# Optimization experiments

Hardware: AMD Instinct MI355X
Metric: run time of the kernel (lower is better)

The kernel has to match this reference:

```python
import jax, jax.numpy as jnp
import numpy as np

N_NODES = 50000
BN_EPS = 1e-5


def graph_conv(x, row, col, ew, n):
    # deg from source indices only (matches torch.bincount(row))
    deg = jnp.zeros((n,), x.dtype).at[row].add(1.0)
    dinv = jnp.where(deg > 0, deg ** -0.5, 0.0)
    norm = dinv[row] * ew * dinv[col]                     # [E]
    msg = norm[:, None] * x[row]                          # [E, F]
    return jax.ops.segment_sum(msg, col, num_segments=n)  # out[dst] += w * x[src]


def batch_norm(x, gamma, beta):
    # training-mode BN over the node (batch) dim, biased variance
    mu = jnp.mean(x, axis=0)
    var = jnp.mean((x - mu) ** 2, axis=0)
    return (x - mu) / jnp.sqrt(var + BN_EPS) * gamma + beta


def setup_inputs() -> dict:
    key = jax.random.key(0)
    ks = jax.random.split(key, 12)
    node_features = jax.random.normal(ks[0], (N_NODES, 100), dtype=jnp.float32)
    edge_index = jax.random.randint(ks[1], (2, 800000), 0, N_NODES, dtype=jnp.int64)
    edge_weights = jax.random.uniform(ks[2], (800000,), dtype=jnp.float32)
    def lin(k, fi, fo):
        lim = 1.0 / np.sqrt(fi)
        k1, k2 = jax.random.split(k)
        W = jax.random.uniform(k1, (fi, fo), minval=-lim, maxval=lim, dtype=jnp.float32)
        b = jax.random.uniform(k2, (fo,), minval=-lim, maxval=lim, dtype=jnp.float32)
        return W, b
    W0, b0 = lin(ks[3], 100, 128)
    W1, b1 = lin(ks[4], 128, 128)
    W2, b2 = lin(ks[5], 128, 64)
    return {
        "node_features": node_features, "edge_index": edge_index, "edge_weights": edge_weights,
        "W0": W0, "b0": b0, "g0": jnp.ones((128,), jnp.float32), "be0": jnp.zeros((128,), jnp.float32),
        "W1": W1, "b1": b1, "g1": jnp.ones((128,), jnp.float32), "be1": jnp.zeros((128,), jnp.float32),
        "W2": W2, "b2": b2,
    }


def reference(node_features, edge_index, edge_weights,
              W0, b0, g0, be0, W1, b1, g1, be1, W2, b2):
    n = node_features.shape[0]
    row, col = edge_index[0], edge_index[1]
    x = node_features
    # layer 0
    x = graph_conv(x, row, col, edge_weights, n)
    x = jax.nn.relu(batch_norm(x @ W0 + b0, g0, be0))
    # layer 1
    x = graph_conv(x, row, col, edge_weights, n)
    x = jax.nn.relu(batch_norm(x @ W1 + b1, g1, be1))
    # final layer (no BN/relu)
    x = graph_conv(x, row, col, edge_weights, n)
    return x @ W2 + b2
```

## Files before the change

kernel.cpp:

```cpp
#include <hip/hip_runtime.h>
#include <cstdint>

#define F0 100
#define FH 128
#define FO 64
#define BN_EPS 1e-5f

typedef unsigned short ushort_t;
typedef unsigned int uint_t;

static inline int ceil_div(long long a, long long b) { return (int)((a + b - 1) / b); }

__device__ __forceinline__ float bf_lo(uint_t w) { return __uint_as_float(w << 16); }
__device__ __forceinline__ float bf_hi(uint_t w) { return __uint_as_float(w & 0xffff0000u); }
__device__ __forceinline__ uint_t f2bf(float f) {
  uint_t u = __float_as_uint(f);
  return (u + 0x7fffu + ((u >> 16) & 1u)) >> 16;
}
__device__ __forceinline__ uint_t pack2(float a, float b) {
  return f2bf(a) | (f2bf(b) << 16);
}


template <int K, int F, int TM, bool BN_A, bool A_BF16, bool OUT_BF16>
__device__ __forceinline__ void gemm2_body(int bid, const void* __restrict__ A_,
                                           const float* __restrict__ W,
                                           const float* __restrict__ bias,
                                           const float* __restrict__ scA,
                                           const float* __restrict__ shA,
                                           void* __restrict__ out_, int n) {
  constexpr int NCG = F / 4;
  constexpr int NRG = 256 / NCG;
  constexpr int BR = NRG * TM;
  constexpr int BK = 32;
  constexpr int F4 = F / 4;

  __shared__ float sW[BK][F];
  __shared__ float sA[BR][BK];

  const int tid = threadIdx.x;
  const int cg = tid % NCG;
  const int rg = tid / NCG;
  const int row0 = bid * BR;

  float4 acc[TM];
#pragma unroll
  for (int t = 0; t < TM; ++t) acc[t] = make_float4(0.f, 0.f, 0.f, 0.f);

  const float4* W4 = (const float4*)W;
  const float4 z4 = make_float4(0.f, 0.f, 0.f, 0.f);

  for (int k0 = 0; k0 < K; k0 += BK) {
    for (int i = tid; i < BK * F4; i += 256) {
      int kk = i / F4, f4 = i % F4;
      int gk = k0 + kk;
      ((float4*)&sW[kk][0])[f4] = (gk < K) ? W4[(size_t)gk * F4 + f4] : z4;
    }
    for (int i = tid; i < BR * (BK / 4); i += 256) {
      int r = i / (BK / 4), k4 = i % (BK / 4);
      int gr = row0 + r;
      int gk = k0 + k4 * 4;
      float4 av = z4;
      if (gr < n && gk + 3 < K) {
        if (A_BF16) {
          uint2 u = ((const uint2*)A_)[(size_t)gr * (K / 4) + (gk >> 2)];
          av.x = bf_lo(u.x); av.y = bf_hi(u.x);
          av.z = bf_lo(u.y); av.w = bf_hi(u.y);
        } else {
          av = ((const float4*)A_)[(size_t)gr * (K / 4) + (gk >> 2)];
        }
        if (BN_A) {
          float4 sc = ((const float4*)scA)[gk >> 2];
          float4 sh = ((const float4*)shA)[gk >> 2];
          av.x = fmaxf(fmaf(av.x, sc.x, sh.x), 0.f);
          av.y = fmaxf(fmaf(av.y, sc.y, sh.y), 0.f);
          av.z = fmaxf(fmaf(av.z, sc.z, sh.z), 0.f);
          av.w = fmaxf(fmaf(av.w, sc.w, sh.w), 0.f);
        }
      }
      ((float4*)&sA[r][0])[k4] = av;
    }
    __syncthreads();
#pragma unroll 4
    for (int kk = 0; kk < BK; ++kk) {
      float4 w = ((const float4*)&sW[kk][0])[cg];
#pragma unroll
      for (int t = 0; t < TM; ++t) {
        float a = sA[rg * TM + t][kk];
        acc[t].x = fmaf(a, w.x, acc[t].x);
        acc[t].y = fmaf(a, w.y, acc[t].y);
        acc[t].z = fmaf(a, w.z, acc[t].z);
        acc[t].w = fmaf(a, w.w, acc[t].w);
      }
    }
    __syncthreads();
  }

  float4 bb = bias ? ((const float4*)bias)[cg] : z4;
#pragma unroll
  for (int t = 0; t < TM; ++t) {
    int gr = row0 + rg * TM + t;
    if (gr < n) {
      float4 v = acc[t];
      v.x += bb.x; v.y += bb.y; v.z += bb.z; v.w += bb.w;
      if (OUT_BF16) {
        ((uint2*)out_)[(size_t)gr * F4 + cg] = make_uint2(pack2(v.x, v.y), pack2(v.z, v.w));
      } else {
        ((float4*)out_)[(size_t)gr * F4 + cg] = v;
      }
    }
  }
}

template <int K, int F, int TM, bool BN_A, bool A_BF16, bool OUT_BF16>
__global__ __launch_bounds__(256) void gemm2_kernel(const void* __restrict__ A,
                                                    const float* __restrict__ W,
                                                    const float* __restrict__ bias,
                                                    const float* __restrict__ scA,
                                                    const float* __restrict__ shA,
                                                    void* __restrict__ out, int n) {
  gemm2_body<K, F, TM, BN_A, A_BF16, OUT_BF16>(blockIdx.x, A, W, bias, scA, shA, out, n);
}


__global__ __launch_bounds__(256) void hist_pos_kernel(const int* __restrict__ row,
                                                       const int* __restrict__ col,
                                                       int* __restrict__ degr,
                                                       int* __restrict__ degc,
                                                       int* __restrict__ posw, int E) {
  int e = blockIdx.x * blockDim.x + threadIdx.x;
  if (e >= E) return;
  atomicAdd(&degr[row[e]], 1);
  posw[e] = atomicAdd(&degc[col[e]], 1);
}


__global__ __launch_bounds__(256) void scan_fused_kernel(const int* __restrict__ degr,
                                                         const int* __restrict__ degc,
                                                         float* __restrict__ dinv,
                                                         int* __restrict__ startp,
                                                         int* __restrict__ bsums, int n) {
  __shared__ int s[256];
  int i = blockIdx.x * 256 + threadIdx.x;
  int dc = 0;
  if (i < n) {
    int dr = degr[i];
    dc = degc[i];
    dinv[i] = (dr > 0) ? rsqrtf((float)dr) : 0.0f;
  }
  s[threadIdx.x] = dc;
  __syncthreads();
  for (int off = 1; off < 256; off <<= 1) {
    int t = 0;
    if (threadIdx.x >= off) t = s[threadIdx.x - off];
    __syncthreads();
    if (threadIdx.x >= off) s[threadIdx.x] += t;
    __syncthreads();
  }
  if (i < n) startp[i] = s[threadIdx.x] - dc;
  if (threadIdx.x == 255) bsums[blockIdx.x] = s[255];
}

__global__ __launch_bounds__(256) void scan_partials_kernel(int* __restrict__ bsums, int nb) {
  __shared__ int s[256];
  int v = (threadIdx.x < nb) ? bsums[threadIdx.x] : 0;
  s[threadIdx.x] = v;
  __syncthreads();
  for (int off = 1; off < 256; off <<= 1) {
    int t = 0;
    if (threadIdx.x >= off) t = s[threadIdx.x - off];
    __syncthreads();
    if (threadIdx.x >= off) s[threadIdx.x] += t;
    __syncthreads();
  }
  if (threadIdx.x < nb) bsums[threadIdx.x] = s[threadIdx.x] - v;
}


__global__ __launch_bounds__(256) void fused_scatter_gemm_kernel(
    const int* __restrict__ row, const int* __restrict__ col, const float* __restrict__ ew,
    const float* __restrict__ dinv, const int* __restrict__ startp,
    const int* __restrict__ bsums, const int* __restrict__ posw, int2* __restrict__ ep, int E,
    const float* __restrict__ A, const float* __restrict__ W, void* __restrict__ out, int n,
    int GB) {
  int bid = blockIdx.x;
  int r5 = bid % 5;
  int g = bid / 5;
  if (r5 == 0 && g < GB) {
    gemm2_body<F0, FH, 8, false, false, true>(g, A, W, nullptr, nullptr, nullptr, out, n);
    return;
  }
  int h = (r5 == 0) ? (bid - GB) : (bid - (g + 1));
  int e = h * 256 + threadIdx.x;
  if (e >= E) return;
  int r = row[e], c = col[e];
  int pos = startp[c] + bsums[c >> 8] + posw[e];
  float coef = dinv[r] * ew[e] * dinv[c];
  ep[pos] = make_int2(r, __float_as_int(coef));
}


template <int F, bool DO_BN, bool OUT_F32>
__global__ __launch_bounds__(256) void conv_bf16_kernel(const ushort_t* __restrict__ x,
                                                        const int* __restrict__ startp,
                                                        const int* __restrict__ bsums,
                                                        const int* __restrict__ degc,
                                                        const int2* __restrict__ ep,
                                                        const float* __restrict__ bias,
                                                        const float* __restrict__ scale,
                                                        const float* __restrict__ shift,
                                                        void* __restrict__ out, int n, int E) {
  constexpr int G2 = F / 8;
  constexpr int TPD = G2 / 2;
  constexpr int DPB = 256 / TPD;
  constexpr int CHUNK = 1024;
  __shared__ int2 eps[CHUNK];

  const int d0 = blockIdx.x * DPB;
  const int dst = d0 + threadIdx.x / TPD;
  const int q = threadIdx.x % TPD;
  const bool valid = dst < n;

  const int blkStart = startp[d0] + bsums[d0 >> 8];
  const int dEnd0 = (d0 + DPB < n) ? (d0 + DPB) : n;
  const int blkEnd = (dEnd0 < n) ? (startp[dEnd0] + bsums[dEnd0 >> 8]) : E;

  int s0 = 0, myEnd = 0;
  if (valid) {
    s0 = startp[dst] + bsums[dst >> 8];
    myEnd = s0 + degc[dst];
  }

  const uint4* x4 = (const uint4*)x;

  float sc[16], sh[16];
  if (DO_BN) {
#pragma unroll
    for (int ch = 0; ch < 2; ++ch) {
      int g = q + ch * TPD;
#pragma unroll
      for (int j = 0; j < 8; ++j) {
        sc[ch * 8 + j] = scale[g * 8 + j];
        sh[ch * 8 + j] = shift[g * 8 + j];
      }
    }
  }

  float acc[16];
#pragma unroll
  for (int j = 0; j < 16; ++j) acc[j] = 0.f;

  for (int cb = blkStart; cb < blkEnd; cb += CHUNK) {
    int cnt = min(CHUNK, blkEnd - cb);
    if (cb != blkStart) __syncthreads();
    for (int i = threadIdx.x; i < cnt; i += 256) eps[i] = ep[cb + i];
    __syncthreads();
    if (valid) {
      int k0 = max(s0, cb);
      int k1 = min(myEnd, cb + cnt);
      for (int k = k0; k < k1; ++k) {
        int2 e = eps[k - cb];
        float c = __int_as_float(e.y);
        const uint4* xp = x4 + (size_t)e.x * G2 + q;
        uint4 v0 = xp[0];
        uint4 v1 = xp[TPD];
        uint_t vv[8] = {v0.x, v0.y, v0.z, v0.w, v1.x, v1.y, v1.z, v1.w};
#pragma unroll
        for (int hh = 0; hh < 8; ++hh) {
          float f0 = bf_lo(vv[hh]);
          float f1 = bf_hi(vv[hh]);
          if (DO_BN) {
            f0 = fmaxf(fmaf(f0, sc[2 * hh], sh[2 * hh]), 0.f);
            f1 = fmaxf(fmaf(f1, sc[2 * hh + 1], sh[2 * hh + 1]), 0.f);
          }
          acc[2 * hh] = fmaf(c, f0, acc[2 * hh]);
          acc[2 * hh + 1] = fmaf(c, f1, acc[2 * hh + 1]);
        }
      }
    }
  }

  if (!valid) return;

  if (bias) {
#pragma unroll
    for (int ch = 0; ch < 2; ++ch) {
      int g = q + ch * TPD;
#pragma unroll
      for (int j = 0; j < 8; ++j) acc[ch * 8 + j] += bias[g * 8 + j];
    }
  }

  if (OUT_F32) {
    float4* o4 = (float4*)out;
    size_t base = (size_t)dst * (F / 4);
    o4[base + 2 * q] = make_float4(acc[0], acc[1], acc[2], acc[3]);
    o4[base + 2 * q + 1] = make_float4(acc[4], acc[5], acc[6], acc[7]);
    o4[base + 2 * (q + TPD)] = make_float4(acc[8], acc[9], acc[10], acc[11]);
    o4[base + 2 * (q + TPD) + 1] = make_float4(acc[12], acc[13], acc[14], acc[15]);
  } else {
    uint4* o4 = (uint4*)out;
    size_t base = (size_t)dst * G2;
    o4[base + q] = make_uint4(pack2(acc[0], acc[1]), pack2(acc[2], acc[3]),
                              pack2(acc[4], acc[5]), pack2(acc[6], acc[7]));
    o4[base + q + TPD] = make_uint4(pack2(acc[8], acc[9]), pack2(acc[10], acc[11]),
                                    pack2(acc[12], acc[13]), pack2(acc[14], acc[15]));
  }
}


__global__ __launch_bounds__(128) void bn_stats_fin_kernel(const ushort_t* __restrict__ z,
                                                           float* __restrict__ sum,
                                                           float* __restrict__ sumsq,
                                                           const float* __restrict__ g,
                                                           const float* __restrict__ be,
                                                           float* __restrict__ scale,
                                                           float* __restrict__ shift,
                                                           int n, int* __restrict__ ctr) {
  int f = threadIdx.x;
  float s = 0.0f, s2 = 0.0f;
  for (int r = blockIdx.x; r < n; r += gridDim.x) {
    float v = __uint_as_float(((uint_t)z[(size_t)r * FH + f]) << 16);
    s += v;
    s2 += v * v;
  }
  unsafeAtomicAdd(&sum[f], s);
  unsafeAtomicAdd(&sumsq[f], s2);
  __threadfence();
  __syncthreads();
  __shared__ int lastFlag;
  if (f == 0) lastFlag = (atomicAdd(ctr, 1) == (int)gridDim.x - 1) ? 1 : 0;
  __syncthreads();
  if (lastFlag) {
    float S = atomicAdd(&sum[f], 0.0f);
    float S2 = atomicAdd(&sumsq[f], 0.0f);
    float invN = 1.0f / (float)n;
    float mean = S * invN;
    float var = fmaxf(S2 * invN - mean * mean, 0.0f);
    float sc = g[f] / sqrtf(var + BN_EPS);
    scale[f] = sc;
    shift[f] = be[f] - mean * sc;
  }
}


extern "C" void kernel_launch(void* const* d_in, const int* in_sizes, int n_in,
                              void* d_out, int out_size, void* d_ws, size_t ws_size,
                              hipStream_t stream) {
  const float* x   = (const float*)d_in[0];
  const int*   ei  = (const int*)d_in[1];
  const float* ew  = (const float*)d_in[2];
  const float* W0  = (const float*)d_in[3];
  const float* b0  = (const float*)d_in[4];
  const float* g0  = (const float*)d_in[5];
  const float* be0 = (const float*)d_in[6];
  const float* W1  = (const float*)d_in[7];
  const float* b1  = (const float*)d_in[8];
  const float* g1  = (const float*)d_in[9];
  const float* be1 = (const float*)d_in[10];
  const float* W2  = (const float*)d_in[11];
  const float* b2  = (const float*)d_in[12];

  const int n = in_sizes[0] / F0;
  const int E = in_sizes[2];
  const int* row = ei;
  const int* col = ei + E;

  ushort_t* bufA  = (ushort_t*)d_ws;
  ushort_t* bufB  = bufA + (size_t)n * FH;
  int2*   ep      = (int2*)(bufB + (size_t)n * FH);
  int*    degc    = (int*)(ep + E);
  int*    degr    = degc + n;
  float*  sum0    = (float*)(degr + n);
  float*  sumsq0  = sum0 + FH;
  float*  sum1    = sumsq0 + FH;
  float*  sumsq1  = sum1 + FH;
  int*    ctr     = (int*)(sumsq1 + FH);
  const size_t zero_bytes = (2 * (size_t)n + 4 * FH + 2) * 4;
  int*    startp  = ctr + 2;
  float*  dinv    = (float*)(startp + n);
  int*    bsums   = (int*)(dinv + n);
  float*  scale0  = (float*)(bsums + 256);
  float*  shift0  = scale0 + FH;
  float*  scale1  = shift0 + FH;
  float*  shift1  = scale1 + FH;
  int*    posw    = (int*)bufB;

  const int nb = ceil_div(n, 256);
  const int GB = ceil_div(n, 64);
  const int HB = ceil_div(E, 256);
  const int CB_H = ceil_div(n, 32);
  const int CB_O = ceil_div(n, 64);

  (void)hipMemsetAsync(degc, 0, zero_bytes, stream);
  hist_pos_kernel<<<HB, 256, 0, stream>>>(row, col, degr, degc, posw, E);
  scan_fused_kernel<<<nb, 256, 0, stream>>>(degr, degc, dinv, startp, bsums, n);
  scan_partials_kernel<<<1, 256, 0, stream>>>(bsums, nb);
  fused_scatter_gemm_kernel<<<GB + HB, 256, 0, stream>>>(row, col, ew, dinv, startp, bsums,
                                                         posw, ep, E, x, W0, bufA, n, GB);

  conv_bf16_kernel<FH, false, false><<<CB_H, 256, 0, stream>>>(
      bufA, startp, bsums, degc, ep, b0, nullptr, nullptr, bufB, n, E);
  bn_stats_fin_kernel<<<256, 128, 0, stream>>>(bufB, sum0, sumsq0, g0, be0, scale0, shift0,
                                               n, ctr + 0);

  conv_bf16_kernel<FH, true, false><<<CB_H, 256, 0, stream>>>(
      bufB, startp, bsums, degc, ep, nullptr, scale0, shift0, bufA, n, E);
  gemm2_kernel<FH, FH, 8, false, true, true><<<GB, 256, 0, stream>>>(
      bufA, W1, b1, nullptr, nullptr, bufB, n);
  bn_stats_fin_kernel<<<256, 128, 0, stream>>>(bufB, sum1, sumsq1, g1, be1, scale1, shift1,
                                               n, ctr + 1);

  gemm2_kernel<FH, FO, 4, true, true, true><<<GB, 256, 0, stream>>>(
      bufB, W2, nullptr, scale1, shift1, bufA, n);
  conv_bf16_kernel<FO, false, true><<<CB_O, 256, 0, stream>>>(
      bufA, startp, bsums, degc, ep, b2, nullptr, nullptr, (float*)d_out, n, E);
}
```

Measured before the change: 406.2 us.

## Fuse aggregation with following GEMM and pad degree counters to reduce contention

New measurement: 409.7 us. About the same (+0.9%).

```diff
diff --git a/kernel.cpp b/kernel.cpp
--- a/kernel.cpp
+++ b/kernel.cpp
@@ -4,6 +4,7 @@
 #define F0 100
 #define FH 128
 #define FO 64
+#define PD 4
 #define BN_EPS 1e-5f
 
 typedef unsigned short ushort_t;
@@ -22,17 +23,14 @@
 }
 
 
-template <int K, int F, int TM, bool BN_A, bool A_BF16, bool OUT_BF16>
+template <int K, int F, int TM, int BK, bool A_BF16, bool OUT_BF16>
 __device__ __forceinline__ void gemm2_body(int bid, const void* __restrict__ A_,
                                            const float* __restrict__ W,
                                            const float* __restrict__ bias,
-                                           const float* __restrict__ scA,
-                                           const float* __restrict__ shA,
                                            void* __restrict__ out_, int n) {
   constexpr int NCG = F / 4;
   constexpr int NRG = 256 / NCG;
   constexpr int BR = NRG * TM;
-  constexpr int BK = 32;
   constexpr int F4 = F / 4;
 
   __shared__ float sW[BK][F];
@@ -69,14 +67,6 @@
         } else {
           av = ((const float4*)A_)[(size_t)gr * (K / 4) + (gk >> 2)];
         }
-        if (BN_A) {
-          float4 sc = ((const float4*)scA)[gk >> 2];
-          float4 sh = ((const float4*)shA)[gk >> 2];
-          av.x = fmaxf(fmaf(av.x, sc.x, sh.x), 0.f);
-          av.y = fmaxf(fmaf(av.y, sc.y, sh.y), 0.f);
-          av.z = fmaxf(fmaf(av.z, sc.z, sh.z), 0.f);
-          av.w = fmaxf(fmaf(av.w, sc.w, sh.w), 0.f);
-        }
       }
       ((float4*)&sA[r][0])[k4] = av;
     }
@@ -112,31 +102,28 @@
   }
 }
 
-template <int K, int F, int TM, bool BN_A, bool A_BF16, bool OUT_BF16>
-__global__ __launch_bounds__(256) void gemm2_kernel(const void* __restrict__ A,
-                                                    const float* __restrict__ W,
-                                                    const float* __restrict__ bias,
-                                                    const float* __restrict__ scA,
-                                                    const float* __restrict__ shA,
-                                                    void* __restrict__ out, int n) {
-  gemm2_body<K, F, TM, BN_A, A_BF16, OUT_BF16>(blockIdx.x, A, W, bias, scA, shA, out, n);
-}
-
-
-__global__ __launch_bounds__(256) void hist_pos_kernel(const int* __restrict__ row,
-                                                       const int* __restrict__ col,
-                                                       int* __restrict__ degr,
-                                                       int* __restrict__ degc,
-                                                       int* __restrict__ posw, int E) {
-  int e = blockIdx.x * blockDim.x + threadIdx.x;
+
+__global__ __launch_bounds__(256) void fused_gemm_hist_kernel(
+    const float* __restrict__ A, const float* __restrict__ W, void* __restrict__ out, int n,
+    int GB, const int* __restrict__ row, const int* __restrict__ col,
+    int* __restrict__ degr_p, int* __restrict__ degc_p, int* __restrict__ posw, int E) {
+  int bid = blockIdx.x;
+  int r5 = bid % 5;
+  int g = bid / 5;
+  if (r5 == 0 && g < GB) {
+    gemm2_body<F0, FH, 8, 16, false, true>(g, A, W, nullptr, out, n);
+    return;
+  }
+  int h = (r5 == 0) ? (bid - GB) : (bid - (g + 1));
+  int e = h * 256 + threadIdx.x;
   if (e >= E) return;
-  atomicAdd(&degr[row[e]], 1);
-  posw[e] = atomicAdd(&degc[col[e]], 1);
-}
-
-
-__global__ __launch_bounds__(256) void scan_fused_kernel(const int* __restrict__ degr,
-                                                         const int* __restrict__ degc,
+  atomicAdd(&degr_p[(size_t)row[e] * PD], 1);
+  posw[e] = atomicAdd(&degc_p[(size_t)col[e] * PD], 1);
+}
+
+
+__global__ __launch_bounds__(256) void scan_fused_kernel(const int* __restrict__ degr_p,
+                                                         const int* __restrict__ degc_p,
                                                          float* __restrict__ dinv,
                                                          int* __restrict__ startp,
                                                          int* __restrict__ bsums, int n) {
@@ -144,8 +131,8 @@
   int i = blockIdx.x * 256 + threadIdx.x;
   int dc = 0;
   if (i < n) {
-    int dr = degr[i];
-    dc = degc[i];
+    int dr = degr_p[(size_t)i * PD];
+    dc = degc_p[(size_t)i * PD];
     dinv[i] = (dr > 0) ? rsqrtf((float)dr) : 0.0f;
   }
   s[threadIdx.x] = dc;
@@ -177,21 +164,15 @@
 }
 
 
-__global__ __launch_bounds__(256) void fused_scatter_gemm_kernel(
-    const int* __restrict__ row, const int* __restrict__ col, const float* __restrict__ ew,
-    const float* __restrict__ dinv, const int* __restrict__ startp,
-    const int* __restrict__ bsums, const int* __restrict__ posw, int2* __restrict__ ep, int E,
-    const float* __restrict__ A, const float* __restrict__ W, void* __restrict__ out, int n,
-    int GB) {
-  int bid = blockIdx.x;
-  int r5 = bid % 5;
-  int g = bid / 5;
-  if (r5 == 0 && g < GB) {
-    gemm2_body<F0, FH, 8, false, false, true>(g, A, W, nullptr, nullptr, nullptr, out, n);
-    return;
-  }
-  int h = (r5 == 0) ? (bid - GB) : (bid - (g + 1));
-  int e = h * 256 + threadIdx.x;
+__global__ __launch_bounds__(256) void csr_scatter2_kernel(const int* __restrict__ row,
+                                                           const int* __restrict__ col,
+                                                           const float* __restrict__ ew,
+                                                           const float* __restrict__ dinv,
+                                                           const int* __restrict__ startp,
+                                                           const int* __restrict__ bsums,
+                                                           const int* __restrict__ posw,
+                                                           int2* __restrict__ ep, int E) {
+  int e = blockIdx.x * blockDim.x + threadIdx.x;
   if (e >= E) return;
   int r = row[e], c = col[e];
   int pos = startp[c] + bsums[c >> 8] + posw[e];
@@ -200,37 +181,14 @@
 }
 
 
-template <int F, bool DO_BN, bool OUT_F32>
-__global__ __launch_bounds__(256) void conv_bf16_kernel(const ushort_t* __restrict__ x,
-                                                        const int* __restrict__ startp,
-                                                        const int* __restrict__ bsums,
-                                                        const int* __restrict__ degc,
-                                                        const int2* __restrict__ ep,
-                                                        const float* __restrict__ bias,
-                                                        const float* __restrict__ scale,
-                                                        const float* __restrict__ shift,
-                                                        void* __restrict__ out, int n, int E) {
-  constexpr int G2 = F / 8;
-  constexpr int TPD = G2 / 2;
-  constexpr int DPB = 256 / TPD;
-  constexpr int CHUNK = 1024;
-  __shared__ int2 eps[CHUNK];
-
-  const int d0 = blockIdx.x * DPB;
-  const int dst = d0 + threadIdx.x / TPD;
-  const int q = threadIdx.x % TPD;
-  const bool valid = dst < n;
-
-  const int blkStart = startp[d0] + bsums[d0 >> 8];
-  const int dEnd0 = (d0 + DPB < n) ? (d0 + DPB) : n;
-  const int blkEnd = (dEnd0 < n) ? (startp[dEnd0] + bsums[dEnd0 >> 8]) : E;
-
-  int s0 = 0, myEnd = 0;
-  if (valid) {
-    s0 = startp[dst] + bsums[dst >> 8];
-    myEnd = s0 + degc[dst];
-  }
-
+template <bool DO_BN>
+__device__ __forceinline__ void conv_accum_128(const ushort_t* __restrict__ x, int s0, int d,
+                                               int q, const int2* __restrict__ ep,
+                                               const float* __restrict__ scale,
+                                               const float* __restrict__ shift,
+                                               float* __restrict__ acc) {
+  constexpr int G2 = FH / 8;
+  constexpr int TPD = 8;
   const uint4* x4 = (const uint4*)x;
 
   float sc[16], sh[16];
@@ -245,66 +203,142 @@
       }
     }
   }
-
+#pragma unroll
+  for (int j = 0; j < 16; ++j) acc[j] = 0.f;
+
+  for (int k = 0; k < d; ++k) {
+    int2 e = ep[s0 + k];
+    float c = __int_as_float(e.y);
+    const uint4* xp = x4 + (size_t)e.x * G2 + q;
+    uint4 v0 = xp[0];
+    uint4 v1 = xp[TPD];
+    uint_t vv[8] = {v0.x, v0.y, v0.z, v0.w, v1.x, v1.y, v1.z, v1.w};
+#pragma unroll
+    for (int hh = 0; hh < 8; ++hh) {
+      float f0 = bf_lo(vv[hh]);
+      float f1 = bf_hi(vv[hh]);
+      if (DO_BN) {
+        f0 = fmaxf(fmaf(f0, sc[2 * hh], sh[2 * hh]), 0.f);
+        f1 = fmaxf(fmaf(f1, sc[2 * hh + 1], sh[2 * hh + 1]), 0.f);
+      }
+      acc[2 * hh] = fmaf(c, f0, acc[2 * hh]);
+      acc[2 * hh + 1] = fmaf(c, f1, acc[2 * hh + 1]);
+    }
+  }
+}
+
+
+__global__ __launch_bounds__(256) void conv0_kernel(const ushort_t* __restrict__ x,
+                                                    const int* __restrict__ startp,
+                                                    const int* __restrict__ bsums,
+                                                    const int* __restrict__ degc_p,
+                                                    const int2* __restrict__ ep,
+                                                    const float* __restrict__ bias,
+                                                    ushort_t* __restrict__ out, int n) {
+  constexpr int TPD = 8;
+  long long tid = (long long)blockIdx.x * 256 + threadIdx.x;
+  if (tid >= (long long)n * TPD) return;
+  int dst = (int)(tid / TPD);
+  int q = (int)(tid % TPD);
+  int s0 = startp[dst] + bsums[dst >> 8];
+  int d = degc_p[(size_t)dst * PD];
   float acc[16];
-#pragma unroll
-  for (int j = 0; j < 16; ++j) acc[j] = 0.f;
-
-  for (int cb = blkStart; cb < blkEnd; cb += CHUNK) {
-    int cnt = min(CHUNK, blkEnd - cb);
-    if (cb != blkStart) __syncthreads();
-    for (int i = threadIdx.x; i < cnt; i += 256) eps[i] = ep[cb + i];
-    __syncthreads();
-    if (valid) {
-      int k0 = max(s0, cb);
-      int k1 = min(myEnd, cb + cnt);
-      for (int k = k0; k < k1; ++k) {
-        int2 e = eps[k - cb];
-        float c = __int_as_float(e.y);
-        const uint4* xp = x4 + (size_t)e.x * G2 + q;
-        uint4 v0 = xp[0];
-        uint4 v1 = xp[TPD];
-        uint_t vv[8] = {v0.x, v0.y, v0.z, v0.w, v1.x, v1.y, v1.z, v1.w};
-#pragma unroll
-        for (int hh = 0; hh < 8; ++hh) {
-          float f0 = bf_lo(vv[hh]);
-          float f1 = bf_hi(vv[hh]);
-          if (DO_BN) {
-            f0 = fmaxf(fmaf(f0, sc[2 * hh], sh[2 * hh]), 0.f);
-            f1 = fmaxf(fmaf(f1, sc[2 * hh + 1], sh[2 * hh + 1]), 0.f);
-          }
-          acc[2 * hh] = fmaf(c, f0, acc[2 * hh]);
-          acc[2 * hh + 1] = fmaf(c, f1, acc[2 * hh + 1]);
-        }
-      }
-    }
-  }
-
-  if (!valid) return;
-
-  if (bias) {
-#pragma unroll
-    for (int ch = 0; ch < 2; ++ch) {
-      int g = q + ch * TPD;
-#pragma unroll
-      for (int j = 0; j < 8; ++j) acc[ch * 8 + j] += bias[g * 8 + j];
-    }
-  }
+  conv_accum_128<false>(x, s0, d, q, ep, nullptr, nullptr, acc);
+#pragma unroll
+  for (int ch = 0; ch < 2; ++ch) {
+    int g = q + ch * TPD;
+#pragma unroll
+    for (int j = 0; j < 8; ++j) acc[ch * 8 + j] += bias[g * 8 + j];
+  }
+  uint4* o4 = (uint4*)out;
+  size_t base = (size_t)dst * (FH / 8);
+  o4[base + q] = make_uint4(pack2(acc[0], acc[1]), pack2(acc[2], acc[3]),
+                            pack2(acc[4], acc[5]), pack2(acc[6], acc[7]));
+  o4[base + q + TPD] = make_uint4(pack2(acc[8], acc[9]), pack2(acc[10], acc[11]),
+                                  pack2(acc[12], acc[13]), pack2(acc[14], acc[15]));
+}
+
+
+template <int FOUT, bool OUT_F32>
+__global__ __launch_bounds__(256) void convgemm_kernel(const ushort_t* __restrict__ x,
+                                                       const int* __restrict__ startp,
+                                                       const int* __restrict__ bsums,
+                                                       const int* __restrict__ degc_p,
+                                                       const int2* __restrict__ ep,
+                                                       const float* __restrict__ scale,
+                                                       const float* __restrict__ shift,
+                                                       const float* __restrict__ W,
+                                                       const float* __restrict__ bias,
+                                                       void* __restrict__ out, int n) {
+  constexpr int TPD = 8;
+  constexpr int BKG = 16;
+  constexpr int CPT = FOUT / 8;
+  __shared__ float sY[32][FH + 1];
+  __shared__ float sW[BKG][FOUT];
+
+  const int tid = threadIdx.x;
+  const int dl = tid / TPD;
+  const int q = tid % TPD;
+  const int dst = blockIdx.x * 32 + dl;
+  const bool valid = dst < n;
+
+  float acc[16];
+  if (valid) {
+    int s0 = startp[dst] + bsums[dst >> 8];
+    int d = degc_p[(size_t)dst * PD];
+    conv_accum_128<true>(x, s0, d, q, ep, scale, shift, acc);
+  } else {
+#pragma unroll
+    for (int j = 0; j < 16; ++j) acc[j] = 0.f;
+  }
+#pragma unroll
+  for (int j = 0; j < 8; ++j) {
+    sY[dl][8 * q + j] = acc[j];
+    sY[dl][64 + 8 * q + j] = acc[8 + j];
+  }
+  __syncthreads();
+
+  const int r = tid / 8;
+  const int cg = tid % 8;
+  float oacc[CPT];
+#pragma unroll
+  for (int j = 0; j < CPT; ++j) oacc[j] = 0.f;
+
+  const float4* W4 = (const float4*)W;
+  for (int k0 = 0; k0 < FH; k0 += BKG) {
+    for (int i = tid; i < BKG * (FOUT / 4); i += 256) {
+      int kk = i / (FOUT / 4), f4 = i % (FOUT / 4);
+      ((float4*)&sW[kk][0])[f4] = W4[(size_t)(k0 + kk) * (FOUT / 4) + f4];
+    }
+    __syncthreads();
+#pragma unroll 4
+    for (int kk = 0; kk < BKG; ++kk) {
+      float a = sY[r][k0 + kk];
+      const float* wrow = &sW[kk][cg * CPT];
+#pragma unroll
+      for (int j = 0; j < CPT; ++j) oacc[j] = fmaf(a, wrow[j], oacc[j]);
+    }
+    __syncthreads();
+  }
+
+  int gr = blockIdx.x * 32 + r;
+  if (gr >= n) return;
+#pragma unroll
+  for (int j = 0; j < CPT; ++j) oacc[j] += bias[cg * CPT + j];
 
   if (OUT_F32) {
     float4* o4 = (float4*)out;
-    size_t base = (size_t)dst * (F / 4);
-    o4[base + 2 * q] = make_float4(acc[0], acc[1], acc[2], acc[3]);
-    o4[base + 2 * q + 1] = make_float4(acc[4], acc[5], acc[6], acc[7]);
-    o4[base + 2 * (q + TPD)] = make_float4(acc[8], acc[9], acc[10], acc[11]);
-    o4[base + 2 * (q + TPD) + 1] = make_float4(acc[12], acc[13], acc[14], acc[15]);
+    size_t base = (size_t)gr * (FOUT / 4) + cg * (CPT / 4);
+#pragma unroll
+    for (int j = 0; j < CPT / 4; ++j)
+      o4[base + j] = make_float4(oacc[4 * j], oacc[4 * j + 1], oacc[4 * j + 2], oacc[4 * j + 3]);
   } else {
-    uint4* o4 = (uint4*)out;
-    size_t base = (size_t)dst * G2;
-    o4[base + q] = make_uint4(pack2(acc[0], acc[1]), pack2(acc[2], acc[3]),
-                              pack2(acc[4], acc[5]), pack2(acc[6], acc[7]));
-    o4[base + q + TPD] = make_uint4(pack2(acc[8], acc[9]), pack2(acc[10], acc[11]),
-                                    pack2(acc[12], acc[13]), pack2(acc[14], acc[15]));
+    uint2* o2 = (uint2*)out;
+    size_t base = (size_t)gr * (FOUT / 4) + cg * (CPT / 4);
+#pragma unroll
+    for (int j = 0; j < CPT / 4; ++j)
+      o2[base + j] = make_uint2(pack2(oacc[4 * j], oacc[4 * j + 1]),
+                                pack2(oacc[4 * j + 2], oacc[4 * j + 3]));
   }
 }
 
@@ -369,14 +403,14 @@
   ushort_t* bufA  = (ushort_t*)d_ws;
   ushort_t* bufB  = bufA + (size_t)n * FH;
   int2*   ep      = (int2*)(bufB + (size_t)n * FH);
-  int*    degc    = (int*)(ep + E);
-  int*    degr    = degc + n;
-  float*  sum0    = (float*)(degr + n);
+  int*    degc_p  = (int*)(ep + E);
+  int*    degr_p  = degc_p + (size_t)n * PD;
+  float*  sum0    = (float*)(degr_p + (size_t)n * PD);
   float*  sumsq0  = sum0 + FH;
   float*  sum1    = sumsq0 + FH;
   float*  sumsq1  = sum1 + FH;
   int*    ctr     = (int*)(sumsq1 + FH);
-  const size_t zero_bytes = (2 * (size_t)n + 4 * FH + 2) * 4;
+  const size_t zero_bytes = (2 * (size_t)n * PD + 4 * FH + 2) * 4;
   int*    startp  = ctr + 2;
   float*  dinv    = (float*)(startp + n);
   int*    bsums   = (int*)(dinv + n);
@@ -389,30 +423,22 @@
   const int nb = ceil_div(n, 256);
   const int GB = ceil_div(n, 64);
   const int HB = ceil_div(E, 256);
-  const int CB_H = ceil_div(n, 32);
-  const int CB_O = ceil_div(n, 64);
-
-  (void)hipMemsetAsync(degc, 0, zero_bytes, stream);
-  hist_pos_kernel<<<HB, 256, 0, stream>>>(row, col, degr, degc, posw, E);
-  scan_fused_kernel<<<nb, 256, 0, stream>>>(degr, degc, dinv, startp, bsums, n);
+  const int CB = ceil_div(n, 32);
+
+  (void)hipMemsetAsync(degc_p, 0, zero_bytes, stream);
+  fused_gemm_hist_kernel<<<GB + HB, 256, 0, stream>>>(x, W0, bufA, n, GB, row, col,
+                                                      degr_p, degc_p, posw, E);
+  scan_fused_kernel<<<nb, 256, 0, stream>>>(degr_p, degc_p, dinv, startp, bsums, n);
   scan_partials_kernel<<<1, 256, 0, stream>>>(bsums, nb);
-  fused_scatter_gemm_kernel<<<GB + HB, 256, 0, stream>>>(row, col, ew, dinv, startp, bsums,
-                                                         posw, ep, E, x, W0, bufA, n, GB);
-
-  conv_bf16_kernel<FH, false, false><<<CB_H, 256, 0, stream>>>(
-      bufA, startp, bsums, degc, ep, b0, nullptr, nullptr, bufB, n, E);
+  csr_scatter2_kernel<<<HB, 256, 0, stream>>>(row, col, ew, dinv, startp, bsums, posw, ep, E);
+
+  conv0_kernel<<<CB, 256, 0, stream>>>(bufA, startp, bsums, degc_p, ep, b0, bufB, n);
   bn_stats_fin_kernel<<<256, 128, 0, stream>>>(bufB, sum0, sumsq0, g0, be0, scale0, shift0,
                                                n, ctr + 0);
-
-  conv_bf16_kernel<FH, true, false><<<CB_H, 256, 0, stream>>>(
-      bufB, startp, bsums, degc, ep, nullptr, scale0, shift0, bufA, n, E);
-  gemm2_kernel<FH, FH, 8, false, true, true><<<GB, 256, 0, stream>>>(
-      bufA, W1, b1, nullptr, nullptr, bufB, n);
-  bn_stats_fin_kernel<<<256, 128, 0, stream>>>(bufB, sum1, sumsq1, g1, be1, scale1, shift1,
+  convgemm_kernel<FH, false><<<CB, 256, 0, stream>>>(bufB, startp, bsums, degc_p, ep,
+                                                     scale0, shift0, W1, b1, bufA, n);
+  bn_stats_fin_kernel<<<256, 128, 0, stream>>>(bufA, sum1, sumsq1, g1, be1, scale1, shift1,
                                                n, ctr + 1);
-
-  gemm2_kernel<FH, FO, 4, true, true, true><<<GB, 256, 0, stream>>>(
-      bufB, W2, nullptr, scale1, shift1, bufA, n);
-  conv_bf16_kernel<FO, false, true><<<CB_O, 256, 0, stream>>>(
-      bufA, startp, bsums, degc, ep, b2, nullptr, nullptr, (float*)d_out, n, E);
-}
+  convgemm_kernel<FO, true><<<CB, 256, 0, stream>>>(bufA, startp, bsums, degc_p, ep,
+                                                    scale1, shift1, W2, b2, (float*)d_out, n);
+}
```
